# Optimization experiments

Measured on AMD Instinct MI355X. Metric: run time of the kernel, lower is better.

## Reference

```python
import jax, jax.numpy as jnp
import numpy as np

H = 128        # hidden_dim
NP = 512       # program nodes
NV = 50000     # voxel nodes
E = 800000     # cross edges (16 per voxel)
TAU = 1.0
SLOPE = 0.01   # LeakyReLU default negative slope


def setup_inputs() -> dict:
    key = jax.random.key(0)
    ks = jax.random.split(key, 12)
    s = 1.0 / np.sqrt(H)
    x = jax.random.normal(ks[0], (NP, H), dtype=jnp.float32)
    v = jax.random.normal(ks[1], (NV, H), dtype=jnp.float32)
    row0 = jax.random.randint(ks[2], (E,), 0, NP, dtype=jnp.int32)
    row1 = (jnp.arange(E, dtype=jnp.int32) % NV)  # every voxel gets E/NV edges
    cross_edge_index = jnp.stack([row0, row1])    # [2, E]
    W_program = jax.random.normal(ks[3], (H, H), dtype=jnp.float32) * s
    b_program = jnp.zeros((H,), dtype=jnp.float32)
    W_voxel = jax.random.normal(ks[4], (H, H), dtype=jnp.float32) * s
    b_voxel = jnp.zeros((H,), dtype=jnp.float32)
    W_m1 = jax.random.normal(ks[5], (H, H), dtype=jnp.float32) * s
    b_m1 = jnp.zeros((H,), dtype=jnp.float32)
    W_m2 = jax.random.normal(ks[6], (H, 1), dtype=jnp.float32) * s
    b_m2 = jnp.zeros((1,), dtype=jnp.float32)
    theta = jax.random.normal(ks[7], (H, 1), dtype=jnp.float32) * s  # xavier-like
    u = jax.random.uniform(ks[8], (E,), dtype=jnp.float32)
    gumbel_u = jnp.clip(u, 1e-7, 1.0 - 1e-7)  # avoid log(0)
    return {"x": x, "v": v, "cross_edge_index": cross_edge_index,
            "W_program": W_program, "b_program": b_program,
            "W_voxel": W_voxel, "b_voxel": b_voxel,
            "W_m1": W_m1, "b_m1": b_m1, "W_m2": W_m2, "b_m2": b_m2,
            "theta": theta, "gumbel_u": gumbel_u}


def reference(x, v, cross_edge_index, W_program, b_program, W_voxel, b_voxel,
              W_m1, b_m1, W_m2, b_m2, theta, gumbel_u):
    src = cross_edge_index[0]
    dst = cross_edge_index[1]
    x_sel = x[src]                      # [E, H] gather
    v_sel = v[dst]                      # [E, H] gather
    # mask = sigmoid(MLP(v)) : Linear -> LeakyReLU -> Linear(H,1)
    a = v @ W_m1 + b_m1
    a = jnp.where(a >= 0, a, SLOPE * a)
    mask = jax.nn.sigmoid(a @ W_m2 + b_m2)                  # [NV, 1]
    # attention logits: theta^T * tanh(Wp x_sel + Wv v_sel), summed over H
    t = jnp.tanh(x_sel @ W_program + b_program + v_sel @ W_voxel + b_voxel)
    e = jnp.sum(t * theta[:, 0], axis=-1)                   # [E]
    # Gumbel softmax: global softmax over all edges (dim=0 in torch on 1-D e)
    g = -jnp.log(-jnp.log(gumbel_u))
    y = jax.nn.softmax((e + g) / TAU)                       # [E]
    # per-voxel hard argmax (scatter_max), straight-through estimator
    seg_max = jax.ops.segment_max(y, dst, num_segments=NV)  # [NV]
    is_max = y == seg_max[dst]
    cand = jnp.where(is_max, jnp.arange(E), E)
    argmax = jax.ops.segment_min(cand, dst, num_segments=NV)  # [NV], first max per voxel
    y_hard_1 = jnp.zeros(E + 1, y.dtype).at[argmax].set(1.0)[:E]  # overflow slot for empty segments
    y_hard = jax.lax.stop_gradient(y_hard_1 - y) + y
    # scatter-sum of soft-attended program features back to voxels
    summed = jax.ops.segment_sum(x_sel * y[:, None], dst, num_segments=NV)  # [NV, H]
    v_out = v + mask * summed
    return (v_out, mask, y[:, None], y_hard[:, None])
```

## Files before the change

kernel.cpp:

```cpp
#include <hip/hip_runtime.h>

#define H     128
#define NP    512
#define NVOX  50000
#define NEDGE 800000
#define EPV   16
#define SLOPE 0.01f
#define GR    32
#define NBLK  1563
#define STRH  136
#define VSTR  132
#define C1    2.8853900817779268f
#define LOG2E 1.4426950408889634f
#define ABLK  3125

#define EXP2(x) __builtin_amdgcn_exp2f(x)
#define LOG2(x) __builtin_amdgcn_logf(x)
#define RCP(x)  __builtin_amdgcn_rcpf(x)

typedef _Float16 h16;
typedef __attribute__((ext_vector_type(4))) _Float16 h16x4;
typedef __attribute__((ext_vector_type(8))) _Float16 h16x8;
typedef __attribute__((ext_vector_type(4))) float    f32x4;

template <int CTRL>
__device__ __forceinline__ float dpp_add(float x) {
    union { float f; int i; } u, r;
    u.f = x;
    r.i = __builtin_amdgcn_update_dpp(0, u.i, CTRL, 0xf, 0xf, true);
    return x + r.f;
}

__global__ __launch_bounds__(256) void k_pre(const float* __restrict__ x,
                                             const float* __restrict__ Wp,
                                             const float* __restrict__ bp,
                                             const float* __restrict__ Wv,
                                             const float* __restrict__ Wm1,
                                             float* __restrict__ xpout,
                                             h16* __restrict__ WvThi,
                                             h16* __restrict__ WvTlo,
                                             h16* __restrict__ Wm1T,
                                             h16* __restrict__ xh) {
    __shared__ float part[H];
    int bid = blockIdx.x;
    int tid = threadIdx.x;
    if (bid < NP) {
        int row = bid;
        int col = tid & 127;
        int kh  = tid >> 7;
        int kbase = kh * 64;
        const float* xr = x + (size_t)row * H;
        float acc = 0.f;
#pragma unroll 8
        for (int k = 0; k < 64; ++k)
            acc = fmaf(xr[kbase + k], Wp[(size_t)(kbase + k) * H + col], acc);
        if (kh == 1) part[col] = acc;
        __syncthreads();
        if (kh == 0) xpout[(size_t)row * H + col] = (acc + part[col] + bp[col]) * C1;
    } else if (bid < NP + 128) {
        int idx = (bid - NP) * 256 + tid;
        if (idx < 16384) {
            int k = idx >> 7, n = idx & 127;
            float w = Wv[idx];
            h16 hi = (h16)w;
            WvThi[n * H + k] = hi;
            WvTlo[n * H + k] = (h16)(w - (float)hi);
        } else {
            int j = idx - 16384;
            int k = j >> 7, n = j & 127;
            Wm1T[n * H + k] = (h16)Wm1[j];
        }
    } else {
        int f4 = (bid - NP - 128) * 256 + tid;
        float4 val = *(const float4*)&x[(size_t)f4 * 4];
        h16x4 hv;
        hv.x = (h16)val.x; hv.y = (h16)val.y;
        hv.z = (h16)val.z; hv.w = (h16)val.w;
        *(h16x4*)&xh[(size_t)f4 * 4] = hv;
    }
}

__global__ __launch_bounds__(256, 4) void k_mainX(
    const float* __restrict__ v,   const h16* __restrict__ xh,
    const float* __restrict__ bv,  const float* __restrict__ bm1,
    const float* __restrict__ Wm2, const float* __restrict__ bm2,
    const h16* __restrict__ WvThi, const h16* __restrict__ WvTlo,
    const h16* __restrict__ Wm1T,
    const float* __restrict__ xp,  const int* __restrict__ cei,
    const float* __restrict__ theta, const float* __restrict__ gum,
    float* __restrict__ mask_out, float* __restrict__ pout,
    float* __restrict__ sump,     float* __restrict__ partial)
{
    __shared__ __align__(16) char ldsbuf[2 * GR * STRH * 2];
    h16*   vh = (h16*)ldsbuf;
    h16*   vl = vh + GR * STRH;
    float* vt = (float*)ldsbuf;
    __shared__ int   ceit[EPV * GR];
    __shared__ float gumt[EPV * GR];
    __shared__ float pmbuf[4][GR];
    __shared__ float psums[4];

    int tid  = threadIdx.x;
    int base = blockIdx.x * GR;

#pragma unroll
    for (int i = 0; i < 4; ++i) {
        int f  = i * 256 + tid;
        int r  = f >> 5, c4 = f & 31;
        int gr = base + r; if (gr >= NVOX) gr = NVOX - 1;
        float4 val = *(const float4*)&v[(size_t)gr * H + c4 * 4];
        h16x4 hi, lo;
        hi.x = (h16)val.x; lo.x = (h16)(val.x - (float)hi.x);
        hi.y = (h16)val.y; lo.y = (h16)(val.y - (float)hi.y);
        hi.z = (h16)val.z; lo.z = (h16)(val.z - (float)hi.z);
        hi.w = (h16)val.w; lo.w = (h16)(val.w - (float)hi.w);
        *(h16x4*)&vh[r * STRH + c4 * 4] = hi;
        *(h16x4*)&vl[r * STRH + c4 * 4] = lo;
    }
#pragma unroll
    for (int it = 0; it < 2; ++it) {
        int idx = it * 256 + tid;
        int t = idx >> 5, c = idx & 31;
        int vx = base + c; if (vx >= NVOX) vx = NVOX - 1;
        int e = vx + t * NVOX;
        ceit[idx] = cei[e];
        gumt[idx] = -LOG2E * RCP(LOG2(gum[e]));
    }
    __syncthreads();

    int wave = tid >> 6, lane = tid & 63;
    int m16 = lane & 15, quad = lane >> 4;
    int cb = wave * 32;

    f32x4 aV[2][2], aM[2][2];
#pragma unroll
    for (int rt = 0; rt < 2; ++rt)
#pragma unroll
        for (int ct = 0; ct < 2; ++ct) { aV[rt][ct] = (f32x4)0.f; aM[rt][ct] = (f32x4)0.f; }

#pragma unroll
    for (int kc = 0; kc < 4; ++kc) {
        int kofs = kc * 32 + quad * 8;
        h16x8 ah[2], al[2];
#pragma unroll
        for (int rt = 0; rt < 2; ++rt) {
            int row = rt * 16 + m16;
            ah[rt] = *(const h16x8*)&vh[row * STRH + kofs];
            al[rt] = *(const h16x8*)&vl[row * STRH + kofs];
        }
#pragma unroll
        for (int ct = 0; ct < 2; ++ct) {
            int n = cb + ct * 16 + m16;
            h16x8 bh = *(const h16x8*)&WvThi[n * H + kofs];
            h16x8 bl = *(const h16x8*)&WvTlo[n * H + kofs];
            h16x8 bm = *(const h16x8*)&Wm1T[n * H + kofs];
#pragma unroll
            for (int rt = 0; rt < 2; ++rt) {
                aV[rt][ct] = __builtin_amdgcn_mfma_f32_16x16x32_f16(ah[rt], bh, aV[rt][ct], 0, 0, 0);
                aV[rt][ct] = __builtin_amdgcn_mfma_f32_16x16x32_f16(al[rt], bh, aV[rt][ct], 0, 0, 0);
                aV[rt][ct] = __builtin_amdgcn_mfma_f32_16x16x32_f16(ah[rt], bl, aV[rt][ct], 0, 0, 0);
                aM[rt][ct] = __builtin_amdgcn_mfma_f32_16x16x32_f16(ah[rt], bm, aM[rt][ct], 0, 0, 0);
            }
        }
    }
    __syncthreads();

    float pml[2][4];
#pragma unroll
    for (int rt = 0; rt < 2; ++rt)
#pragma unroll
        for (int reg = 0; reg < 4; ++reg) pml[rt][reg] = 0.f;
#pragma unroll
    for (int ct = 0; ct < 2; ++ct) {
        int col = cb + ct * 16 + m16;
        float bvc = bv[col], bmc = bm1[col], w2c = Wm2[col];
#pragma unroll
        for (int rt = 0; rt < 2; ++rt)
#pragma unroll
            for (int reg = 0; reg < 4; ++reg) {
                int row = rt * 16 + quad * 4 + reg;
                vt[row * VSTR + col] = (aV[rt][ct][reg] + bvc) * C1;
                float m = aM[rt][ct][reg] + bmc;
                m = (m >= 0.f) ? m : SLOPE * m;
                pml[rt][reg] = fmaf(m, w2c, pml[rt][reg]);
            }
    }
#pragma unroll
    for (int rt = 0; rt < 2; ++rt)
#pragma unroll
        for (int reg = 0; reg < 4; ++reg) {
            pml[rt][reg] = dpp_add<0xB1>(pml[rt][reg]);
            pml[rt][reg] = dpp_add<0x4E>(pml[rt][reg]);
            pml[rt][reg] = dpp_add<0x141>(pml[rt][reg]);
            pml[rt][reg] = dpp_add<0x140>(pml[rt][reg]);
        }
    if (m16 == 0) {
#pragma unroll
        for (int rt = 0; rt < 2; ++rt)
#pragma unroll
            for (int reg = 0; reg < 4; ++reg)
                pmbuf[wave][rt * 16 + quad * 4 + reg] = pml[rt][reg];
    }
    __syncthreads();
    if (wave == 0 && lane < GR) {
        int gr = base + lane;
        if (gr < NVOX) {
            float s = pmbuf[0][lane] + pmbuf[1][lane] + pmbuf[2][lane]
                    + pmbuf[3][lane] + bm2[0];
            mask_out[gr] = RCP(1.f + EXP2(-s * LOG2E));
        }
    }

    int g = tid >> 3, lk = tid & 7;
    int vox = base + g;
    bool valid = vox < NVOX;
    float th2[16], thsum = 0.f;
#pragma unroll
    for (int i = 0; i < 4; ++i) {
        float4 t4 = *(const float4*)&theta[(lk + 8 * i) * 4];
        th2[i * 4 + 0] = -2.f * LOG2E * t4.x; th2[i * 4 + 1] = -2.f * LOG2E * t4.y;
        th2[i * 4 + 2] = -2.f * LOG2E * t4.z; th2[i * 4 + 3] = -2.f * LOG2E * t4.w;
        thsum += LOG2E * (t4.x + t4.y + t4.z + t4.w);
    }
    const float* vr = &vt[g * VSTR];
    float4 b0 = *(const float4*)&vr[(lk +  0) * 4];
    float4 b1 = *(const float4*)&vr[(lk +  8) * 4];
    float4 b2 = *(const float4*)&vr[(lk + 16) * 4];
    float4 b3 = *(const float4*)&vr[(lk + 24) * 4];

    float4 s0a = make_float4(0.f,0.f,0.f,0.f), s0b = s0a, s1a = s0a, s1b = s0a;
    float psum = 0.f, pmax = -1.f;
    int   pidx = 0;

    int src0 = ceit[g];
    const float4* r0 = (const float4*)(xp + (size_t)src0 * H);
    float4 a0 = r0[lk], a1 = r0[lk + 8], a2 = r0[lk + 16], a3 = r0[lk + 24];
    const h16x8* q0 = (const h16x8*)(xh + (size_t)src0 * H);
    h16x8 c0 = q0[lk], c1 = q0[lk + 8];

    for (int t = 0; t < EPV; ++t) {
        float4 n0, n1, n2, n3;
        h16x8 d0, d1;
        int srcN;
        if (t < EPV - 1) {
            srcN = ceit[(t + 1) * GR + g];
            const float4* rN = (const float4*)(xp + (size_t)srcN * H);
            n0 = rN[lk]; n1 = rN[lk + 8]; n2 = rN[lk + 16]; n3 = rN[lk + 24];
            const h16x8* qN = (const h16x8*)(xh + (size_t)srcN * H);
            d0 = qN[lk]; d1 = qN[lk + 8];
        } else {
            srcN = src0; n0 = a0; n1 = a1; n2 = a2; n3 = a3;
            d0 = c0; d1 = c1;
        }
        float wvt = gumt[t * GR + g];

        float acc0 = thsum, acc1 = 0.f;
        acc0 = fmaf(th2[ 0], RCP(EXP2(a0.x + b0.x) + 1.f), acc0);
        acc1 = fmaf(th2[ 1], RCP(EXP2(a0.y + b0.y) + 1.f), acc1);
        acc0 = fmaf(th2[ 2], RCP(EXP2(a0.z + b0.z) + 1.f), acc0);
        acc1 = fmaf(th2[ 3], RCP(EXP2(a0.w + b0.w) + 1.f), acc1);
        acc0 = fmaf(th2[ 4], RCP(EXP2(a1.x + b1.x) + 1.f), acc0);
        acc1 = fmaf(th2[ 5], RCP(EXP2(a1.y + b1.y) + 1.f), acc1);
        acc0 = fmaf(th2[ 6], RCP(EXP2(a1.z + b1.z) + 1.f), acc0);
        acc1 = fmaf(th2[ 7], RCP(EXP2(a1.w + b1.w) + 1.f), acc1);
        acc0 = fmaf(th2[ 8], RCP(EXP2(a2.x + b2.x) + 1.f), acc0);
        acc1 = fmaf(th2[ 9], RCP(EXP2(a2.y + b2.y) + 1.f), acc1);
        acc0 = fmaf(th2[10], RCP(EXP2(a2.z + b2.z) + 1.f), acc0);
        acc1 = fmaf(th2[11], RCP(EXP2(a2.w + b2.w) + 1.f), acc1);
        acc0 = fmaf(th2[12], RCP(EXP2(a3.x + b3.x) + 1.f), acc0);
        acc1 = fmaf(th2[13], RCP(EXP2(a3.y + b3.y) + 1.f), acc1);
        acc0 = fmaf(th2[14], RCP(EXP2(a3.z + b3.z) + 1.f), acc0);
        acc1 = fmaf(th2[15], RCP(EXP2(a3.w + b3.w) + 1.f), acc1);
        float acc = acc0 + acc1;
        acc = dpp_add<0xB1>(acc);
        acc = dpp_add<0x4E>(acc);
        acc = dpp_add<0x141>(acc);
        float p = EXP2(acc) * wvt;
        if (p > pmax) { pmax = p; pidx = t; }
        if (valid) psum += p;
        if (lk == 0 && valid) pout[vox + t * NVOX] = p;
        s0a.x = fmaf(p, (float)c0[0], s0a.x); s0a.y = fmaf(p, (float)c0[1], s0a.y);
        s0a.z = fmaf(p, (float)c0[2], s0a.z); s0a.w = fmaf(p, (float)c0[3], s0a.w);
        s0b.x = fmaf(p, (float)c0[4], s0b.x); s0b.y = fmaf(p, (float)c0[5], s0b.y);
        s0b.z = fmaf(p, (float)c0[6], s0b.z); s0b.w = fmaf(p, (float)c0[7], s0b.w);
        s1a.x = fmaf(p, (float)c1[0], s1a.x); s1a.y = fmaf(p, (float)c1[1], s1a.y);
        s1a.z = fmaf(p, (float)c1[2], s1a.z); s1a.w = fmaf(p, (float)c1[3], s1a.w);
        s1b.x = fmaf(p, (float)c1[4], s1b.x); s1b.y = fmaf(p, (float)c1[5], s1b.y);
        s1b.z = fmaf(p, (float)c1[6], s1b.z); s1b.w = fmaf(p, (float)c1[7], s1b.w);
        a0 = n0; a1 = n1; a2 = n2; a3 = n3;
        c0 = d0; c1 = d1;
        src0 = srcN;
    }
    if (lk == 0 && valid) pout[vox + pidx * NVOX] = -pmax;
    if (valid) {
        float* sr = sump + (size_t)vox * H;
        *(float4*)&sr[lk * 8]          = s0a;
        *(float4*)&sr[lk * 8 + 4]      = s0b;
        *(float4*)&sr[64 + lk * 8]     = s1a;
        *(float4*)&sr[64 + lk * 8 + 4] = s1b;
    }
    psum += __shfl_xor(psum, 8, 64);
    psum += __shfl_xor(psum, 16, 64);
    psum += __shfl_xor(psum, 32, 64);
    if (lane == 0) psums[wave] = psum;
    __syncthreads();
    if (tid == 0)
        partial[blockIdx.x] = psums[0] + psums[1] + psums[2] + psums[3];
}

__global__ __launch_bounds__(256) void k_out(const float* __restrict__ v,
                                             const float* __restrict__ maskp,
                                             const float* __restrict__ partial,
                                             float* __restrict__ vout,
                                             float* __restrict__ ybuf,
                                             float* __restrict__ yhard) {
    __shared__ float wsum[4];
    int tid = threadIdx.x;
    float s = 0.f;
    for (int i = tid; i < NBLK; i += 256) s += partial[i];
#pragma unroll
    for (int off = 32; off >= 1; off >>= 1) s += __shfl_xor(s, off, 64);
    if ((tid & 63) == 0) wsum[tid >> 6] = s;
    __syncthreads();
    float invS = RCP(wsum[0] + wsum[1] + wsum[2] + wsum[3]);

    int bid = blockIdx.x;
    if (bid < ABLK) {
#pragma unroll
        for (int r = 0; r < 2; ++r) {
            int i = (bid + r * ABLK) * 256 + tid;
            float4 sp = ((const float4*)vout)[i];
            float4 vv = ((const float4*)v)[i];
            float  m  = maskp[i >> 5] * invS;
            float4 o;
            o.x = fmaf(m, sp.x, vv.x); o.y = fmaf(m, sp.y, vv.y);
            o.z = fmaf(m, sp.z, vv.z); o.w = fmaf(m, sp.w, vv.w);
            ((float4*)vout)[i] = o;
        }
    } else {
        int e = (bid - ABLK) * 256 + tid;
        float pv = ybuf[e];
        ybuf[e]  = fabsf(pv) * invS;
        yhard[e] = (pv < 0.f) ? 1.f : 0.f;
    }
}

extern "C" void kernel_launch(void* const* d_in, const int* in_sizes, int n_in,
                              void* d_out, int out_size, void* d_ws, size_t ws_size,
                              hipStream_t stream) {
    (void)in_sizes; (void)n_in; (void)out_size; (void)ws_size;
    const float* x   = (const float*)d_in[0];
    const float* v   = (const float*)d_in[1];
    const int*   cei = (const int*)d_in[2];
    const float* Wp  = (const float*)d_in[3];
    const float* bp  = (const float*)d_in[4];
    const float* Wv  = (const float*)d_in[5];
    const float* bv  = (const float*)d_in[6];
    const float* Wm1 = (const float*)d_in[7];
    const float* bm1 = (const float*)d_in[8];
    const float* Wm2 = (const float*)d_in[9];
    const float* bm2 = (const float*)d_in[10];
    const float* th  = (const float*)d_in[11];
    const float* gum = (const float*)d_in[12];

    float* out   = (float*)d_out;
    float* vout  = out;
    float* maskp = out + (size_t)NVOX * H;
    float* ybuf  = maskp + NVOX;
    float* yhard = ybuf + NEDGE;
    float* xp    = yhard;
    h16*   WvThi = (h16*)(yhard + 65536);
    h16*   WvTlo = WvThi + 16384;
    h16*   Wm1T  = WvThi + 32768;
    h16*   xh    = WvThi + 49152;
    float* partial = (float*)d_ws;

    k_pre<<<NP + 192, 256, 0, stream>>>(x, Wp, bp, Wv, Wm1, xp, WvThi, WvTlo,
                                        Wm1T, xh);
    k_mainX<<<NBLK, 256, 0, stream>>>(v, xh, bv, bm1, Wm2, bm2, WvThi, WvTlo,
                                      Wm1T, xp, cei, th, gum, maskp, ybuf, vout,
                                      partial);
    k_out<<<2 * ABLK, 256, 0, stream>>>(v, maskp, partial, vout, ybuf, yhard);
}
```

Measured before the change: 178.4 us.

## Split fused GEMM+edge kernel into separate GEMM and edge kernels via workspace

```diff
diff --git a/kernel.cpp b/kernel.cpp
--- a/kernel.cpp
+++ b/kernel.cpp
@@ -80,25 +80,19 @@
     }
 }
 
-__global__ __launch_bounds__(256, 4) void k_mainX(
-    const float* __restrict__ v,   const h16* __restrict__ xh,
-    const float* __restrict__ bv,  const float* __restrict__ bm1,
-    const float* __restrict__ Wm2, const float* __restrict__ bm2,
+__global__ __launch_bounds__(256, 4) void k_gemm(
+    const float* __restrict__ v,   const float* __restrict__ bv,
+    const float* __restrict__ bm1, const float* __restrict__ Wm2,
+    const float* __restrict__ bm2,
     const h16* __restrict__ WvThi, const h16* __restrict__ WvTlo,
     const h16* __restrict__ Wm1T,
-    const float* __restrict__ xp,  const int* __restrict__ cei,
-    const float* __restrict__ theta, const float* __restrict__ gum,
-    float* __restrict__ mask_out, float* __restrict__ pout,
-    float* __restrict__ sump,     float* __restrict__ partial)
+    float* __restrict__ mask_out,  float* __restrict__ vtg)
 {
     __shared__ __align__(16) char ldsbuf[2 * GR * STRH * 2];
     h16*   vh = (h16*)ldsbuf;
     h16*   vl = vh + GR * STRH;
     float* vt = (float*)ldsbuf;
-    __shared__ int   ceit[EPV * GR];
-    __shared__ float gumt[EPV * GR];
     __shared__ float pmbuf[4][GR];
-    __shared__ float psums[4];
 
     int tid  = threadIdx.x;
     int base = blockIdx.x * GR;
@@ -117,6 +111,114 @@
         *(h16x4*)&vh[r * STRH + c4 * 4] = hi;
         *(h16x4*)&vl[r * STRH + c4 * 4] = lo;
     }
+    __syncthreads();
+
+    int wave = tid >> 6, lane = tid & 63;
+    int m16 = lane & 15, quad = lane >> 4;
+    int cb = wave * 32;
+
+    f32x4 aV[2][2], aM[2][2];
+#pragma unroll
+    for (int rt = 0; rt < 2; ++rt)
+#pragma unroll
+        for (int ct = 0; ct < 2; ++ct) { aV[rt][ct] = (f32x4)0.f; aM[rt][ct] = (f32x4)0.f; }
+
+#pragma unroll
+    for (int kc = 0; kc < 4; ++kc) {
+        int kofs = kc * 32 + quad * 8;
+        h16x8 ah[2], al[2];
+#pragma unroll
+        for (int rt = 0; rt < 2; ++rt) {
+            int row = rt * 16 + m16;
+            ah[rt] = *(const h16x8*)&vh[row * STRH + kofs];
+            al[rt] = *(const h16x8*)&vl[row * STRH + kofs];
+        }
+#pragma unroll
+        for (int ct = 0; ct < 2; ++ct) {
+            int n = cb + ct * 16 + m16;
+            h16x8 bh = *(const h16x8*)&WvThi[n * H + kofs];
+            h16x8 bl = *(const h16x8*)&WvTlo[n * H + kofs];
+            h16x8 bm = *(const h16x8*)&Wm1T[n * H + kofs];
+#pragma unroll
+            for (int rt = 0; rt < 2; ++rt) {
+                aV[rt][ct] = __builtin_amdgcn_mfma_f32_16x16x32_f16(ah[rt], bh, aV[rt][ct], 0, 0, 0);
+                aV[rt][ct] = __builtin_amdgcn_mfma_f32_16x16x32_f16(al[rt], bh, aV[rt][ct], 0, 0, 0);
+                aV[rt][ct] = __builtin_amdgcn_mfma_f32_16x16x32_f16(ah[rt], bl, aV[rt][ct], 0, 0, 0);
+                aM[rt][ct] = __builtin_amdgcn_mfma_f32_16x16x32_f16(ah[rt], bm, aM[rt][ct], 0, 0, 0);
+            }
+        }
+    }
+    __syncthreads();
+
+    float pml[2][4];
+#pragma unroll
+    for (int rt = 0; rt < 2; ++rt)
+#pragma unroll
+        for (int reg = 0; reg < 4; ++reg) pml[rt][reg] = 0.f;
+#pragma unroll
+    for (int ct = 0; ct < 2; ++ct) {
+        int col = cb + ct * 16 + m16;
+        float bvc = bv[col], bmc = bm1[col], w2c = Wm2[col];
+#pragma unroll
+        for (int rt = 0; rt < 2; ++rt)
+#pragma unroll
+            for (int reg = 0; reg < 4; ++reg) {
+                int row = rt * 16 + quad * 4 + reg;
+                vt[row * VSTR + col] = (aV[rt][ct][reg] + bvc) * C1;
+                float m = aM[rt][ct][reg] + bmc;
+                m = (m >= 0.f) ? m : SLOPE * m;
+                pml[rt][reg] = fmaf(m, w2c, pml[rt][reg]);
+            }
+    }
+#pragma unroll
+    for (int rt = 0; rt < 2; ++rt)
+#pragma unroll
+        for (int reg = 0; reg < 4; ++reg) {
+            pml[rt][reg] = dpp_add<0xB1>(pml[rt][reg]);
+            pml[rt][reg] = dpp_add<0x4E>(pml[rt][reg]);
+            pml[rt][reg] = dpp_add<0x141>(pml[rt][reg]);
+            pml[rt][reg] = dpp_add<0x140>(pml[rt][reg]);
+        }
+    if (m16 == 0) {
+#pragma unroll
+        for (int rt = 0; rt < 2; ++rt)
+#pragma unroll
+            for (int reg = 0; reg < 4; ++reg)
+                pmbuf[wave][rt * 16 + quad * 4 + reg] = pml[rt][reg];
+    }
+    __syncthreads();
+    if (wave == 0 && lane < GR) {
+        int gr = base + lane;
+        if (gr < NVOX) {
+            float s = pmbuf[0][lane] + pmbuf[1][lane] + pmbuf[2][lane]
+                    + pmbuf[3][lane] + bm2[0];
+            mask_out[gr] = RCP(1.f + EXP2(-s * LOG2E));
+        }
+    }
+#pragma unroll
+    for (int i = 0; i < 4; ++i) {
+        int f  = i * 256 + tid;
+        int r  = f >> 5, c4 = f & 31;
+        int gr = base + r;
+        if (gr < NVOX)
+            *(float4*)&vtg[(size_t)gr * H + c4 * 4] =
+                *(const float4*)&vt[r * VSTR + c4 * 4];
+    }
+}
+
+__global__ __launch_bounds__(256, 4) void k_edge(
+    const h16* __restrict__ xh,   const float* __restrict__ xp,
+    const int* __restrict__ cei,  const float* __restrict__ theta,
+    const float* __restrict__ gum, const float* __restrict__ vtg,
+    float* __restrict__ pout,     float* __restrict__ sump,
+    float* __restrict__ partial)
+{
+    __shared__ int   ceit[EPV * GR];
+    __shared__ float gumt[EPV * GR];
+    __shared__ float psums[4];
+
+    int tid  = threadIdx.x;
+    int base = blockIdx.x * GR;
 #pragma unroll
     for (int it = 0; it < 2; ++it) {
         int idx = it * 256 + tid;
@@ -129,91 +231,11 @@
     __syncthreads();
 
     int wave = tid >> 6, lane = tid & 63;
-    int m16 = lane & 15, quad = lane >> 4;
-    int cb = wave * 32;
-
-    f32x4 aV[2][2], aM[2][2];
-#pragma unroll
-    for (int rt = 0; rt < 2; ++rt)
-#pragma unroll
-        for (int ct = 0; ct < 2; ++ct) { aV[rt][ct] = (f32x4)0.f; aM[rt][ct] = (f32x4)0.f; }
-
-#pragma unroll
-    for (int kc = 0; kc < 4; ++kc) {
-        int kofs = kc * 32 + quad * 8;
-        h16x8 ah[2], al[2];
-#pragma unroll
-        for (int rt = 0; rt < 2; ++rt) {
-            int row = rt * 16 + m16;
-            ah[rt] = *(const h16x8*)&vh[row * STRH + kofs];
-            al[rt] = *(const h16x8*)&vl[row * STRH + kofs];
-        }
-#pragma unroll
-        for (int ct = 0; ct < 2; ++ct) {
-            int n = cb + ct * 16 + m16;
-            h16x8 bh = *(const h16x8*)&WvThi[n * H + kofs];
-            h16x8 bl = *(const h16x8*)&WvTlo[n * H + kofs];
-            h16x8 bm = *(const h16x8*)&Wm1T[n * H + kofs];
-#pragma unroll
-            for (int rt = 0; rt < 2; ++rt) {
-                aV[rt][ct] = __builtin_amdgcn_mfma_f32_16x16x32_f16(ah[rt], bh, aV[rt][ct], 0, 0, 0);
-                aV[rt][ct] = __builtin_amdgcn_mfma_f32_16x16x32_f16(al[rt], bh, aV[rt][ct], 0, 0, 0);
-                aV[rt][ct] = __builtin_amdgcn_mfma_f32_16x16x32_f16(ah[rt], bl, aV[rt][ct], 0, 0, 0);
-                aM[rt][ct] = __builtin_amdgcn_mfma_f32_16x16x32_f16(ah[rt], bm, aM[rt][ct], 0, 0, 0);
-            }
-        }
-    }
-    __syncthreads();
-
-    float pml[2][4];
-#pragma unroll
-    for (int rt = 0; rt < 2; ++rt)
-#pragma unroll
-        for (int reg = 0; reg < 4; ++reg) pml[rt][reg] = 0.f;
-#pragma unroll
-    for (int ct = 0; ct < 2; ++ct) {
-        int col = cb + ct * 16 + m16;
-        float bvc = bv[col], bmc = bm1[col], w2c = Wm2[col];
-#pragma unroll
-        for (int rt = 0; rt < 2; ++rt)
-#pragma unroll
-            for (int reg = 0; reg < 4; ++reg) {
-                int row = rt * 16 + quad * 4 + reg;
-                vt[row * VSTR + col] = (aV[rt][ct][reg] + bvc) * C1;
-                float m = aM[rt][ct][reg] + bmc;
-                m = (m >= 0.f) ? m : SLOPE * m;
-                pml[rt][reg] = fmaf(m, w2c, pml[rt][reg]);
-            }
-    }
-#pragma unroll
-    for (int rt = 0; rt < 2; ++rt)
-#pragma unroll
-        for (int reg = 0; reg < 4; ++reg) {
-            pml[rt][reg] = dpp_add<0xB1>(pml[rt][reg]);
-            pml[rt][reg] = dpp_add<0x4E>(pml[rt][reg]);
-            pml[rt][reg] = dpp_add<0x141>(pml[rt][reg]);
-            pml[rt][reg] = dpp_add<0x140>(pml[rt][reg]);
-        }
-    if (m16 == 0) {
-#pragma unroll
-        for (int rt = 0; rt < 2; ++rt)
-#pragma unroll
-            for (int reg = 0; reg < 4; ++reg)
-                pmbuf[wave][rt * 16 + quad * 4 + reg] = pml[rt][reg];
-    }
-    __syncthreads();
-    if (wave == 0 && lane < GR) {
-        int gr = base + lane;
-        if (gr < NVOX) {
-            float s = pmbuf[0][lane] + pmbuf[1][lane] + pmbuf[2][lane]
-                    + pmbuf[3][lane] + bm2[0];
-            mask_out[gr] = RCP(1.f + EXP2(-s * LOG2E));
-        }
-    }
-
     int g = tid >> 3, lk = tid & 7;
     int vox = base + g;
     bool valid = vox < NVOX;
+    int voxc = valid ? vox : (NVOX - 1);
+
     float th2[16], thsum = 0.f;
 #pragma unroll
     for (int i = 0; i < 4; ++i) {
@@ -222,11 +244,8 @@
         th2[i * 4 + 2] = -2.f * LOG2E * t4.z; th2[i * 4 + 3] = -2.f * LOG2E * t4.w;
         thsum += LOG2E * (t4.x + t4.y + t4.z + t4.w);
     }
-    const float* vr = &vt[g * VSTR];
-    float4 b0 = *(const float4*)&vr[(lk +  0) * 4];
-    float4 b1 = *(const float4*)&vr[(lk +  8) * 4];
-    float4 b2 = *(const float4*)&vr[(lk + 16) * 4];
-    float4 b3 = *(const float4*)&vr[(lk + 24) * 4];
+    const float4* vr = (const float4*)(vtg + (size_t)voxc * H);
+    float4 b0 = vr[lk], b1 = vr[lk + 8], b2 = vr[lk + 16], b3 = vr[lk + 24];
 
     float4 s0a = make_float4(0.f,0.f,0.f,0.f), s0b = s0a, s1a = s0a, s1b = s0a;
     float psum = 0.f, pmax = -1.f;
@@ -308,6 +327,234 @@
         partial[blockIdx.x] = psums[0] + psums[1] + psums[2] + psums[3];
 }
 
+__global__ __launch_bounds__(256, 4) void k_mainX(
+    const float* __restrict__ v,   const h16* __restrict__ xh,
+    const float* __restrict__ bv,  const float* __restrict__ bm1,
+    const float* __restrict__ Wm2, const float* __restrict__ bm2,
+    const h16* __restrict__ WvThi, const h16* __restrict__ WvTlo,
+    const h16* __restrict__ Wm1T,
+    const float* __restrict__ xp,  const int* __restrict__ cei,
+    const float* __restrict__ theta, const float* __restrict__ gum,
+    float* __restrict__ mask_out, float* __restrict__ pout,
+    float* __restrict__ sump,     float* __restrict__ partial)
+{
+    __shared__ __align__(16) char ldsbuf[2 * GR * STRH * 2];
+    h16*   vh = (h16*)ldsbuf;
+    h16*   vl = vh + GR * STRH;
+    float* vt = (float*)ldsbuf;
+    __shared__ int   ceit[EPV * GR];
+    __shared__ float gumt[EPV * GR];
+    __shared__ float pmbuf[4][GR];
+    __shared__ float psums[4];
+
+    int tid  = threadIdx.x;
+    int base = blockIdx.x * GR;
+
+#pragma unroll
+    for (int i = 0; i < 4; ++i) {
+        int f  = i * 256 + tid;
+        int r  = f >> 5, c4 = f & 31;
+        int gr = base + r; if (gr >= NVOX) gr = NVOX - 1;
+        float4 val = *(const float4*)&v[(size_t)gr * H + c4 * 4];
+        h16x4 hi, lo;
+        hi.x = (h16)val.x; lo.x = (h16)(val.x - (float)hi.x);
+        hi.y = (h16)val.y; lo.y = (h16)(val.y - (float)hi.y);
+        hi.z = (h16)val.z; lo.z = (h16)(val.z - (float)hi.z);
+        hi.w = (h16)val.w; lo.w = (h16)(val.w - (float)hi.w);
+        *(h16x4*)&vh[r * STRH + c4 * 4] = hi;
+        *(h16x4*)&vl[r * STRH + c4 * 4] = lo;
+    }
+#pragma unroll
+    for (int it = 0; it < 2; ++it) {
+        int idx = it * 256 + tid;
+        int t = idx >> 5, c = idx & 31;
+        int vx = base + c; if (vx >= NVOX) vx = NVOX - 1;
+        int e = vx + t * NVOX;
+        ceit[idx] = cei[e];
+        gumt[idx] = -LOG2E * RCP(LOG2(gum[e]));
+    }
+    __syncthreads();
+
+    int wave = tid >> 6, lane = tid & 63;
+    int m16 = lane & 15, quad = lane >> 4;
+    int cb = wave * 32;
+
+    f32x4 aV[2][2], aM[2][2];
+#pragma unroll
+    for (int rt = 0; rt < 2; ++rt)
+#pragma unroll
+        for (int ct = 0; ct < 2; ++ct) { aV[rt][ct] = (f32x4)0.f; aM[rt][ct] = (f32x4)0.f; }
+
+#pragma unroll
+    for (int kc = 0; kc < 4; ++kc) {
+        int kofs = kc * 32 + quad * 8;
+        h16x8 ah[2], al[2];
+#pragma unroll
+        for (int rt = 0; rt < 2; ++rt) {
+            int row = rt * 16 + m16;
+            ah[rt] = *(const h16x8*)&vh[row * STRH + kofs];
+            al[rt] = *(const h16x8*)&vl[row * STRH + kofs];
+        }
+#pragma unroll
+        for (int ct = 0; ct < 2; ++ct) {
+            int n = cb + ct * 16 + m16;
+            h16x8 bh = *(const h16x8*)&WvThi[n * H + kofs];
+            h16x8 bl = *(const h16x8*)&WvTlo[n * H + kofs];
+            h16x8 bm = *(const h16x8*)&Wm1T[n * H + kofs];
+#pragma unroll
+            for (int rt = 0; rt < 2; ++rt) {
+                aV[rt][ct] = __builtin_amdgcn_mfma_f32_16x16x32_f16(ah[rt], bh, aV[rt][ct], 0, 0, 0);
+                aV[rt][ct] = __builtin_amdgcn_mfma_f32_16x16x32_f16(al[rt], bh, aV[rt][ct], 0, 0, 0);
+                aV[rt][ct] = __builtin_amdgcn_mfma_f32_16x16x32_f16(ah[rt], bl, aV[rt][ct], 0, 0, 0);
+                aM[rt][ct] = __builtin_amdgcn_mfma_f32_16x16x32_f16(ah[rt], bm, aM[rt][ct], 0, 0, 0);
+            }
+        }
+    }
+    __syncthreads();
+
+    float pml[2][4];
+#pragma unroll
+    for (int rt = 0; rt < 2; ++rt)
+#pragma unroll
+        for (int reg = 0; reg < 4; ++reg) pml[rt][reg] = 0.f;
+#pragma unroll
+    for (int ct = 0; ct < 2; ++ct) {
+        int col = cb + ct * 16 + m16;
+        float bvc = bv[col], bmc = bm1[col], w2c = Wm2[col];
+#pragma unroll
+        for (int rt = 0; rt < 2; ++rt)
+#pragma unroll
+            for (int reg = 0; reg < 4; ++reg) {
+                int row = rt * 16 + quad * 4 + reg;
+                vt[row * VSTR + col] = (aV[rt][ct][reg] + bvc) * C1;
+                float m = aM[rt][ct][reg] + bmc;
+                m = (m >= 0.f) ? m : SLOPE * m;
+                pml[rt][reg] = fmaf(m, w2c, pml[rt][reg]);
+            }
+    }
+#pragma unroll
+    for (int rt = 0; rt < 2; ++rt)
+#pragma unroll
+        for (int reg = 0; reg < 4; ++reg) {
+            pml[rt][reg] = dpp_add<0xB1>(pml[rt][reg]);
+            pml[rt][reg] = dpp_add<0x4E>(pml[rt][reg]);
+            pml[rt][reg] = dpp_add<0x141>(pml[rt][reg]);
+            pml[rt][reg] = dpp_add<0x140>(pml[rt][reg]);
+        }
+    if (m16 == 0) {
+#pragma unroll
+        for (int rt = 0; rt < 2; ++rt)
+#pragma unroll
+            for (int reg = 0; reg < 4; ++reg)
+                pmbuf[wave][rt * 16 + quad * 4 + reg] = pml[rt][reg];
+    }
+    __syncthreads();
+    if (wave == 0 && lane < GR) {
+        int gr = base + lane;
+        if (gr < NVOX) {
+            float s = pmbuf[0][lane] + pmbuf[1][lane] + pmbuf[2][lane]
+                    + pmbuf[3][lane] + bm2[0];
+            mask_out[gr] = RCP(1.f + EXP2(-s * LOG2E));
+        }
+    }
+
+    int g = tid >> 3, lk = tid & 7;
+    int vox = base + g;
+    bool valid = vox < NVOX;
+    float th2[16], thsum = 0.f;
+#pragma unroll
+    for (int i = 0; i < 4; ++i) {
+        float4 t4 = *(const float4*)&theta[(lk + 8 * i) * 4];
+        th2[i * 4 + 0] = -2.f * LOG2E * t4.x; th2[i * 4 + 1] = -2.f * LOG2E * t4.y;
+        th2[i * 4 + 2] = -2.f * LOG2E * t4.z; th2[i * 4 + 3] = -2.f * LOG2E * t4.w;
+        thsum += LOG2E * (t4.x + t4.y + t4.z + t4.w);
+    }
+    const float* vrr = &vt[g * VSTR];
+    float4 b0 = *(const float4*)&vrr[(lk +  0) * 4];
+    float4 b1 = *(const float4*)&vrr[(lk +  8) * 4];
+    float4 b2 = *(const float4*)&vrr[(lk + 16) * 4];
+    float4 b3 = *(const float4*)&vrr[(lk + 24) * 4];
+
+    float4 s0a = make_float4(0.f,0.f,0.f,0.f), s0b = s0a, s1a = s0a, s1b = s0a;
+    float psum = 0.f, pmax = -1.f;
+    int   pidx = 0;
+
+    int src0 = ceit[g];
+    const float4* r0 = (const float4*)(xp + (size_t)src0 * H);
+    float4 a0 = r0[lk], a1 = r0[lk + 8], a2 = r0[lk + 16], a3 = r0[lk + 24];
+    const h16x8* q0 = (const h16x8*)(xh + (size_t)src0 * H);
+    h16x8 c0 = q0[lk], c1 = q0[lk + 8];
+
+    for (int t = 0; t < EPV; ++t) {
+        float4 n0, n1, n2, n3;
+        h16x8 d0, d1;
+        int srcN;
+        if (t < EPV - 1) {
+            srcN = ceit[(t + 1) * GR + g];
+            const float4* rN = (const float4*)(xp + (size_t)srcN * H);
+            n0 = rN[lk]; n1 = rN[lk + 8]; n2 = rN[lk + 16]; n3 = rN[lk + 24];
+            const h16x8* qN = (const h16x8*)(xh + (size_t)srcN * H);
+            d0 = qN[lk]; d1 = qN[lk + 8];
+        } else {
+            srcN = src0; n0 = a0; n1 = a1; n2 = a2; n3 = a3;
+            d0 = c0; d1 = c1;
+        }
+        float wvt = gumt[t * GR + g];
+
+        float acc0 = thsum, acc1 = 0.f;
+        acc0 = fmaf(th2[ 0], RCP(EXP2(a0.x + b0.x) + 1.f), acc0);
+        acc1 = fmaf(th2[ 1], RCP(EXP2(a0.y + b0.y) + 1.f), acc1);
+        acc0 = fmaf(th2[ 2], RCP(EXP2(a0.z + b0.z) + 1.f), acc0);
+        acc1 = fmaf(th2[ 3], RCP(EXP2(a0.w + b0.w) + 1.f), acc1);
+        acc0 = fmaf(th2[ 4], RCP(EXP2(a1.x + b1.x) + 1.f), acc0);
+        acc1 = fmaf(th2[ 5], RCP(EXP2(a1.y + b1.y) + 1.f), acc1);
+        acc0 = fmaf(th2[ 6], RCP(EXP2(a1.z + b1.z) + 1.f), acc0);
+        acc1 = fmaf(th2[ 7], RCP(EXP2(a1.w + b1.w) + 1.f), acc1);
+        acc0 = fmaf(th2[ 8], RCP(EXP2(a2.x + b2.x) + 1.f), acc0);
+        acc1 = fmaf(th2[ 9], RCP(EXP2(a2.y + b2.y) + 1.f), acc1);
+        acc0 = fmaf(th2[10], RCP(EXP2(a2.z + b2.z) + 1.f), acc0);
+        acc1 = fmaf(th2[11], RCP(EXP2(a2.w + b2.w) + 1.f), acc1);
+        acc0 = fmaf(th2[12], RCP(EXP2(a3.x + b3.x) + 1.f), acc0);
+        acc1 = fmaf(th2[13], RCP(EXP2(a3.y + b3.y) + 1.f), acc1);
+        acc0 = fmaf(th2[14], RCP(EXP2(a3.z + b3.z) + 1.f), acc0);
+        acc1 = fmaf(th2[15], RCP(EXP2(a3.w + b3.w) + 1.f), acc1);
+        float acc = acc0 + acc1;
+        acc = dpp_add<0xB1>(acc);
+        acc = dpp_add<0x4E>(acc);
+        acc = dpp_add<0x141>(acc);
+        float p = EXP2(acc) * wvt;
+        if (p > pmax) { pmax = p; pidx = t; }
+        if (valid) psum += p;
+        if (lk == 0 && valid) pout[vox + t * NVOX] = p;
+        s0a.x = fmaf(p, (float)c0[0], s0a.x); s0a.y = fmaf(p, (float)c0[1], s0a.y);
+        s0a.z = fmaf(p, (float)c0[2], s0a.z); s0a.w = fmaf(p, (float)c0[3], s0a.w);
+        s0b.x = fmaf(p, (float)c0[4], s0b.x); s0b.y = fmaf(p, (float)c0[5], s0b.y);
+        s0b.z = fmaf(p, (float)c0[6], s0b.z); s0b.w = fmaf(p, (float)c0[7], s0b.w);
+        s1a.x = fmaf(p, (float)c1[0], s1a.x); s1a.y = fmaf(p, (float)c1[1], s1a.y);
+        s1a.z = fmaf(p, (float)c1[2], s1a.z); s1a.w = fmaf(p, (float)c1[3], s1a.w);
+        s1b.x = fmaf(p, (float)c1[4], s1b.x); s1b.y = fmaf(p, (float)c1[5], s1b.y);
+        s1b.z = fmaf(p, (float)c1[6], s1b.z); s1b.w = fmaf(p, (float)c1[7], s1b.w);
+        a0 = n0; a1 = n1; a2 = n2; a3 = n3;
+        c0 = d0; c1 = d1;
+        src0 = srcN;
+    }
+    if (lk == 0 && valid) pout[vox + pidx * NVOX] = -pmax;
+    if (valid) {
+        float* sr = sump + (size_t)vox * H;
+        *(float4*)&sr[lk * 8]          = s0a;
+        *(float4*)&sr[lk * 8 + 4]      = s0b;
+        *(float4*)&sr[64 + lk * 8]     = s1a;
+        *(float4*)&sr[64 + lk * 8 + 4] = s1b;
+    }
+    psum += __shfl_xor(psum, 8, 64);
+    psum += __shfl_xor(psum, 16, 64);
+    psum += __shfl_xor(psum, 32, 64);
+    if (lane == 0) psums[wave] = psum;
+    __syncthreads();
+    if (tid == 0)
+        partial[blockIdx.x] = psums[0] + psums[1] + psums[2] + psums[3];
+}
+
 __global__ __launch_bounds__(256) void k_out(const float* __restrict__ v,
                                              const float* __restrict__ maskp,
                                              const float* __restrict__ partial,
@@ -348,7 +595,7 @@
 extern "C" void kernel_launch(void* const* d_in, const int* in_sizes, int n_in,
                               void* d_out, int out_size, void* d_ws, size_t ws_size,
                               hipStream_t stream) {
-    (void)in_sizes; (void)n_in; (void)out_size; (void)ws_size;
+    (void)in_sizes; (void)n_in; (void)out_size;
     const float* x   = (const float*)d_in[0];
     const float* v   = (const float*)d_in[1];
     const int*   cei = (const int*)d_in[2];
@@ -374,11 +621,21 @@
     h16*   Wm1T  = WvThi + 32768;
     h16*   xh    = WvThi + 49152;
     float* partial = (float*)d_ws;
+    float* vtg   = (float*)((char*)d_ws + 8192);
+
+    size_t need = 8192 + (size_t)NVOX * H * sizeof(float);
 
     k_pre<<<NP + 192, 256, 0, stream>>>(x, Wp, bp, Wv, Wm1, xp, WvThi, WvTlo,
                                         Wm1T, xh);
-    k_mainX<<<NBLK, 256, 0, stream>>>(v, xh, bv, bm1, Wm2, bm2, WvThi, WvTlo,
-                                      Wm1T, xp, cei, th, gum, maskp, ybuf, vout,
-                                      partial);
+    if (ws_size >= need) {
+        k_gemm<<<NBLK, 256, 0, stream>>>(v, bv, bm1, Wm2, bm2, WvThi, WvTlo,
+                                         Wm1T, maskp, vtg);
+        k_edge<<<NBLK, 256, 0, stream>>>(xh, xp, cei, th, gum, vtg,
+                                         ybuf, vout, partial);
+    } else {
+        k_mainX<<<NBLK, 256, 0, stream>>>(v, xh, bv, bm1, Wm2, bm2, WvThi,
+                                          WvTlo, Wm1T, xp, cei, th, gum,
+                                          maskp, ybuf, vout, partial);
+    }
     k_out<<<2 * ABLK, 256, 0, stream>>>(v, maskp, partial, vout, ybuf, yhard);
 }
```

Result: slower. 187.5 us (+5.1%).
